# Kernel optimization log

Measured on AMD Instinct MI355X. Metric: run time of the kernel, lower is better.

Reference implementation:

```python
import jax, jax.numpy as jnp
import numpy as np

D_IN, L, D, K, N_CLASSES = 1024, 512, 384, 1, 2

def setup_inputs() -> dict:
    key = jax.random.key(0)
    ks = jax.random.split(key, 11)
    x = jax.random.normal(ks[0], (2, 40000, D_IN), dtype=jnp.float32)
    # Linear params stored as [in, out]; xavier-normal-ish scale
    def w(k, i, o):
        return jax.random.normal(k, (i, o), dtype=jnp.float32) * jnp.sqrt(2.0 / (i + o))
    return {
        "x": x,
        "Wf": w(ks[1], D_IN, L), "bf": jnp.zeros((L,), jnp.float32),
        "Wa": w(ks[2], L, D),    "ba": jnp.zeros((D,), jnp.float32),
        "Wb": w(ks[3], L, D),    "bb": jnp.zeros((D,), jnp.float32),
        "Wc": w(ks[4], D, K),    "bc": jnp.zeros((K,), jnp.float32),
        "Wcls": w(ks[5], L * K, N_CLASSES), "bcls": jnp.zeros((N_CLASSES,), jnp.float32),
    }

def reference(x, Wf, bf, Wa, ba, Wb, bb, Wc, bc, Wcls, bcls):
    # feature embed: Linear + ReLU  (mil_norm=None -> Identity norms)
    h = jax.nn.relu(jnp.einsum('bnd,de->bne', x, Wf) + bf)   # [B,N,L]
    # gated attention
    a = jnp.tanh(jnp.einsum('bnl,ld->bnd', h, Wa) + ba)      # [B,N,D]
    g = jax.nn.sigmoid(jnp.einsum('bnl,ld->bnd', h, Wb) + bb)
    s = jnp.einsum('bnd,dk->bnk', a * g, Wc) + bc            # [B,N,K]
    A = jax.nn.softmax(jnp.swapaxes(s, -1, -2), axis=-1)     # [B,K,N]
    pooled = jnp.einsum('bkn,bnl->bkl', A, h)                # [B,K,L]
    logits = jnp.squeeze(pooled, 1) @ Wcls + bcls            # [B,n_classes]
    return logits
```

## Files before the change

kernel.cpp:

```cpp
#include <hip/hip_runtime.h>
#include <cstdint>

typedef _Float16 f16;
typedef __attribute__((ext_vector_type(8))) _Float16 half8;
typedef __attribute__((ext_vector_type(4))) float floatx4;

#define NB      40000
#define M_TOTAL 80000
#define DIN     1024
#define LDIM    512
#define NBLK    1250
#define BPB     625
#define NCHUNK  16
#define RCHUNK  40

__global__ void k_prep(const float* __restrict__ Wf, const float* __restrict__ Wa,
                       const float* __restrict__ Wb,
                       f16* __restrict__ packedF, f16* __restrict__ packedAB)
{
    const int gid = blockIdx.x * 256 + threadIdx.x;
    if (gid < 65536) {
        const int lq = gid & 3, n = (gid >> 2) & 511, kb = gid >> 11;
        const int kbase = kb * 32 + lq * 8;
        half8 v;
        #pragma unroll
        for (int j = 0; j < 8; ++j) v[j] = (f16)Wf[(kbase + j) * 512 + n];
        *(half8*)&packedF[(long)gid * 8] = v;
    } else if (gid < 65536 + 49152) {
        const int g = gid - 65536;
        const int kb = g / 3072;
        const int rem = g - kb * 3072;
        const int c = rem >> 2, lq = rem & 3;
        const int d = ((c >> 5) << 4) + (c & 15);
        const int type = (c >> 4) & 1;
        const float* src = type ? Wb : Wa;
        const int kbase = kb * 32 + lq * 8;
        half8 v;
        #pragma unroll
        for (int j = 0; j < 8; ++j) v[j] = (f16)src[(kbase + j) * 384 + d];
        *(half8*)&packedAB[(long)g * 8] = v;
    }
}

__device__ inline float fast_sigmoid(float xx) { return 1.0f / (1.0f + __expf(-xx)); }
__device__ inline float fast_tanh(float xx) {
    float e = __expf(-2.0f * fabsf(xx));
    float r = (1.0f - e) / (1.0f + e);
    return xx >= 0.0f ? r : -r;
}

__global__ __launch_bounds__(512, 4) void k_fused(
    const float* __restrict__ x, const f16* __restrict__ packedF,
    const f16* __restrict__ packedAB,
    const float* __restrict__ bf, const float* __restrict__ ba,
    const float* __restrict__ bb, const float* __restrict__ Wc,
    float* __restrict__ partial_pool, float* __restrict__ partial_denom)
{
    __shared__ __align__(16) f16 Hs[64][512];
    __shared__ __align__(16) f16 As[64][128];
    float* wbuf = (float*)&As[0][0];

    const int tid = threadIdx.x;
    const int w = tid >> 6, lane = tid & 63, lr = lane & 15, lq = lane >> 4;
    const long row0 = (long)blockIdx.x * 64;
    const int sr = tid >> 3;
    const int sc = (tid & 7) << 4;
    const int swzw = (sr & 7) << 3;
    const int swzr = (lr & 7) << 3;
    const float* xp = x + (row0 + sr) * DIN + sc;

    floatx4 acc[4][4] = {};
    float4 xr0 = *(const float4*)xp;
    float4 xr1 = *(const float4*)(xp + 4);
    float4 xr2 = *(const float4*)(xp + 8);
    float4 xr3 = *(const float4*)(xp + 12);
    for (int kt = 0; kt < 8; ++kt) {
        if (kt) __syncthreads();
        {
            half8 v0, v1;
            v0[0]=(f16)xr0.x; v0[1]=(f16)xr0.y; v0[2]=(f16)xr0.z; v0[3]=(f16)xr0.w;
            v0[4]=(f16)xr1.x; v0[5]=(f16)xr1.y; v0[6]=(f16)xr1.z; v0[7]=(f16)xr1.w;
            v1[0]=(f16)xr2.x; v1[1]=(f16)xr2.y; v1[2]=(f16)xr2.z; v1[3]=(f16)xr2.w;
            v1[4]=(f16)xr3.x; v1[5]=(f16)xr3.y; v1[6]=(f16)xr3.z; v1[7]=(f16)xr3.w;
            *(half8*)&As[sr][sc ^ swzw] = v0;
            *(half8*)&As[sr][(sc + 8) ^ swzw] = v1;
        }
        __syncthreads();
        if (kt < 7) {
            const float* q = xp + (kt + 1) * 128;
            xr0 = *(const float4*)q;
            xr1 = *(const float4*)(q + 4);
            xr2 = *(const float4*)(q + 8);
            xr3 = *(const float4*)(q + 12);
        }
        #pragma unroll
        for (int kq = 0; kq < 4; ++kq) {
            const int kb = kt * 4 + kq;
            half8 bfr[4];
            #pragma unroll
            for (int tj = 0; tj < 4; ++tj)
                bfr[tj] = *(const half8*)&packedF[(long)((kb * 512 + w * 64 + tj * 16 + lr) << 5) + lq * 8];
            half8 af[4];
            #pragma unroll
            for (int ti = 0; ti < 4; ++ti)
                af[ti] = *(const half8*)&As[ti * 16 + lr][(kq * 32 + lq * 8) ^ swzr];
            #pragma unroll
            for (int tj = 0; tj < 4; ++tj)
                #pragma unroll
                for (int ti = 0; ti < 4; ++ti)
                    acc[ti][tj] = __builtin_amdgcn_mfma_f32_16x16x32_f16(af[ti], bfr[tj], acc[ti][tj], 0, 0, 0);
        }
    }
    #pragma unroll
    for (int tj = 0; tj < 4; ++tj) {
        const int col = w * 64 + tj * 16 + lr;
        const float bias = bf[col];
        #pragma unroll
        for (int ti = 0; ti < 4; ++ti)
            #pragma unroll
            for (int r = 0; r < 4; ++r) {
                const int row = ti * 16 + lq * 4 + r;
                Hs[row][col ^ ((row & 7) << 3)] = (f16)fmaxf(acc[ti][tj][r] + bias, 0.0f);
            }
    }
    __syncthreads();
    if (tid < 64) wbuf[tid] = 0.0f;
    __syncthreads();

    floatx4 acc2[4][6] = {};
    for (int kb = 0; kb < 16; ++kb) {
        half8 af[4];
        #pragma unroll
        for (int ti = 0; ti < 4; ++ti)
            af[ti] = *(const half8*)&Hs[ti * 16 + lr][(kb * 32 + lq * 8) ^ swzr];
        #pragma unroll
        for (int tj = 0; tj < 6; ++tj) {
            half8 bfr = *(const half8*)&packedAB[(long)((kb * 768 + w * 96 + tj * 16 + lr) << 5) + lq * 8];
            #pragma unroll
            for (int ti = 0; ti < 4; ++ti)
                acc2[ti][tj] = __builtin_amdgcn_mfma_f32_16x16x32_f16(af[ti], bfr, acc2[ti][tj], 0, 0, 0);
        }
    }
    float sp[4][4] = {};
    #pragma unroll
    for (int u = 0; u < 3; ++u) {
        const int d = w * 48 + u * 16 + lr;
        const float biasA = ba[d], biasB = bb[d], wcv = Wc[d];
        #pragma unroll
        for (int ti = 0; ti < 4; ++ti)
            #pragma unroll
            for (int r = 0; r < 4; ++r) {
                const float av = fast_tanh(acc2[ti][2 * u][r] + biasA);
                const float gv = fast_sigmoid(acc2[ti][2 * u + 1][r] + biasB);
                sp[ti][r] += av * gv * wcv;
            }
    }
    #pragma unroll
    for (int m = 1; m < 16; m <<= 1)
        #pragma unroll
        for (int ti = 0; ti < 4; ++ti)
            #pragma unroll
            for (int r = 0; r < 4; ++r)
                sp[ti][r] += __shfl_xor(sp[ti][r], m, 64);
    if (lr == 0) {
        #pragma unroll
        for (int ti = 0; ti < 4; ++ti)
            #pragma unroll
            for (int r = 0; r < 4; ++r)
                atomicAdd(&wbuf[ti * 16 + lq * 4 + r], sp[ti][r]);
    }
    __syncthreads();
    if (tid < 64) wbuf[tid] = __expf(wbuf[tid]);
    __syncthreads();

    {
        const int c = tid;
        float pacc = 0.0f;
        #pragma unroll 8
        for (int n = 0; n < 64; ++n)
            pacc += wbuf[n] * (float)Hs[n][c ^ ((n & 7) << 3)];
        partial_pool[(long)blockIdx.x * 512 + c] = pacc;
    }
    if (w == 0) {
        float dsum = wbuf[lane];
        #pragma unroll
        for (int o = 32; o > 0; o >>= 1) dsum += __shfl_xor(dsum, o, 64);
        if (lane == 0) partial_denom[blockIdx.x] = dsum;
    }
}

__global__ __launch_bounds__(512) void k_reduce1(
    const float* __restrict__ pp, const float* __restrict__ pd,
    float* __restrict__ pp2, float* __restrict__ pd2)
{
    __shared__ float dsh[8];
    const int b = blockIdx.x >> 4, chunk = blockIdx.x & 15;
    const int tid = threadIdx.x;
    const int r0 = chunk * RCHUNK;
    const int rows = (BPB - r0 < RCHUNK) ? (BPB - r0) : RCHUNK;
    const float* base = pp + ((long)b * BPB + r0) * 512 + tid;
    float acc = 0.0f;
    for (int i = 0; i < rows; ++i) acc += base[(long)i * 512];
    pp2[((long)b * NCHUNK + chunk) * 512 + tid] = acc;
    float d = 0.0f;
    for (int i = tid; i < rows; i += 512) d += pd[b * BPB + r0 + i];
    #pragma unroll
    for (int o = 32; o > 0; o >>= 1) d += __shfl_xor(d, o, 64);
    if ((tid & 63) == 0) dsh[tid >> 6] = d;
    __syncthreads();
    if (tid == 0)
        pd2[b * NCHUNK + chunk] = dsh[0] + dsh[1] + dsh[2] + dsh[3]
                                + dsh[4] + dsh[5] + dsh[6] + dsh[7];
}

__global__ __launch_bounds__(512) void k_reduce2(
    const float* __restrict__ pp2, const float* __restrict__ pd2,
    const float* __restrict__ Wcls, const float* __restrict__ bcls,
    float* __restrict__ out)
{
    __shared__ float pooled[512];
    __shared__ float dsh[8];
    const int b = blockIdx.x, tid = threadIdx.x;
    float acc = 0.0f;
    const float* base = pp2 + (long)b * NCHUNK * 512 + tid;
    #pragma unroll
    for (int i = 0; i < NCHUNK; ++i) acc += base[i * 512];
    pooled[tid] = acc;
    float d = (tid < NCHUNK) ? pd2[b * NCHUNK + tid] : 0.0f;
    #pragma unroll
    for (int o = 32; o > 0; o >>= 1) d += __shfl_xor(d, o, 64);
    if ((tid & 63) == 0) dsh[tid >> 6] = d;
    __syncthreads();
    const float denom = dsh[0] + dsh[1] + dsh[2] + dsh[3] + dsh[4] + dsh[5] + dsh[6] + dsh[7];
    if (tid < 128) {
        const int cls = tid >> 6, ln = tid & 63;
        float sum = 0.0f;
        #pragma unroll
        for (int t = 0; t < 8; ++t)
            sum += pooled[t * 64 + ln] * Wcls[(t * 64 + ln) * 2 + cls];
        #pragma unroll
        for (int o = 32; o > 0; o >>= 1) sum += __shfl_xor(sum, o, 64);
        if (ln == 0) out[b * 2 + cls] = sum / denom + bcls[cls];
    }
}

extern "C" void kernel_launch(void* const* d_in, const int* in_sizes, int n_in,
                              void* d_out, int out_size, void* d_ws, size_t ws_size,
                              hipStream_t stream)
{
    const float* x    = (const float*)d_in[0];
    const float* Wf   = (const float*)d_in[1];
    const float* bf   = (const float*)d_in[2];
    const float* Wa   = (const float*)d_in[3];
    const float* ba   = (const float*)d_in[4];
    const float* Wb   = (const float*)d_in[5];
    const float* bb   = (const float*)d_in[6];
    const float* Wc   = (const float*)d_in[7];
    const float* Wcls = (const float*)d_in[9];
    const float* bcls = (const float*)d_in[10];
    float* out = (float*)d_out;

    char* w = (char*)d_ws;
    f16*   packedF  = (f16*)(w);
    f16*   packedAB = (f16*)(w + 1048576);
    float* ppool    = (float*)(w + 1835008);
    float* pdenom   = (float*)(w + 4395008);
    float* pp2      = (float*)(w);
    float* pd2      = (float*)(w + 65536);

    k_prep   <<<448, 256, 0, stream>>>(Wf, Wa, Wb, packedF, packedAB);
    k_fused  <<<NBLK, 512, 0, stream>>>(x, packedF, packedAB, bf, ba, bb, Wc, ppool, pdenom);
    k_reduce1<<<32, 512, 0, stream>>>(ppool, pdenom, pp2, pd2);
    k_reduce2<<<2, 512, 0, stream>>>(pp2, pd2, Wcls, bcls, out);
}
```

Baseline: 690.3 us.

## Double fused-kernel row tile to 128 with 16 waves sharing weight fragments

Each fused block now handles 128 rows instead of 64, using 1024 threads arranged as a 2x8 grid of waves. Both row halves reuse the same column slices of the packed Wf/Wa/Wb weights, which cuts weight fetch traffic per row. Blocks are now mapped per batch, so each batch's final block has only 64 valid rows; it clamps loads and zeroes the weights of the missing rows. Pool and denominator partials are still written in 64-row halves so the reduction stage's layout is kept. Costs: LDS per block doubles to about 160KB, the grid is coarser with a possible tail effect, and register pressure under the new launch bounds rises.

```diff
diff --git a/kernel.cpp b/kernel.cpp
--- a/kernel.cpp
+++ b/kernel.cpp
@@ -6,11 +6,12 @@
 typedef __attribute__((ext_vector_type(4))) float floatx4;
 
 #define NB      40000
-#define M_TOTAL 80000
 #define DIN     1024
 #define LDIM    512
-#define NBLK    1250
-#define BPB     625
+#define BLKM    128
+#define BPBATCH 313
+#define GRID_F  626
+#define BPB     626
 #define NCHUNK  16
 #define RCHUNK  40
 
@@ -49,25 +50,33 @@
     return xx >= 0.0f ? r : -r;
 }
 
-__global__ __launch_bounds__(512, 4) void k_fused(
+__global__ __launch_bounds__(1024, 4) void k_fused(
     const float* __restrict__ x, const f16* __restrict__ packedF,
     const f16* __restrict__ packedAB,
     const float* __restrict__ bf, const float* __restrict__ ba,
     const float* __restrict__ bb, const float* __restrict__ Wc,
     float* __restrict__ partial_pool, float* __restrict__ partial_denom)
 {
-    __shared__ __align__(16) f16 Hs[64][512];
-    __shared__ __align__(16) f16 As[64][128];
+    __shared__ __align__(16) f16 Hs[128][512];
+    __shared__ __align__(16) f16 As[128][128];
     float* wbuf = (float*)&As[0][0];
 
     const int tid = threadIdx.x;
     const int w = tid >> 6, lane = tid & 63, lr = lane & 15, lq = lane >> 4;
-    const long row0 = (long)blockIdx.x * 64;
+    const int wm = w & 1;
+    const int wc = w >> 1;
+    const int bid = blockIdx.x;
+    const int batch = (bid >= BPBATCH) ? 1 : 0;
+    const int blk = bid - batch * BPBATCH;
+    const long row0 = (long)batch * NB + (long)blk * BLKM;
+    const int nvalid = (blk == BPBATCH - 1) ? 64 : BLKM;
+
     const int sr = tid >> 3;
     const int sc = (tid & 7) << 4;
     const int swzw = (sr & 7) << 3;
     const int swzr = (lr & 7) << 3;
-    const float* xp = x + (row0 + sr) * DIN + sc;
+    const long srow = row0 + (sr < nvalid ? sr : nvalid - 1);
+    const float* xp = x + srow * DIN + sc;
 
     floatx4 acc[4][4] = {};
     float4 xr0 = *(const float4*)xp;
@@ -99,11 +108,11 @@
             half8 bfr[4];
             #pragma unroll
             for (int tj = 0; tj < 4; ++tj)
-                bfr[tj] = *(const half8*)&packedF[(long)((kb * 512 + w * 64 + tj * 16 + lr) << 5) + lq * 8];
+                bfr[tj] = *(const half8*)&packedF[(long)((kb * 512 + wc * 64 + tj * 16 + lr) << 5) + lq * 8];
             half8 af[4];
             #pragma unroll
             for (int ti = 0; ti < 4; ++ti)
-                af[ti] = *(const half8*)&As[ti * 16 + lr][(kq * 32 + lq * 8) ^ swzr];
+                af[ti] = *(const half8*)&As[wm * 64 + ti * 16 + lr][(kq * 32 + lq * 8) ^ swzr];
             #pragma unroll
             for (int tj = 0; tj < 4; ++tj)
                 #pragma unroll
@@ -113,18 +122,18 @@
     }
     #pragma unroll
     for (int tj = 0; tj < 4; ++tj) {
-        const int col = w * 64 + tj * 16 + lr;
+        const int col = wc * 64 + tj * 16 + lr;
         const float bias = bf[col];
         #pragma unroll
         for (int ti = 0; ti < 4; ++ti)
             #pragma unroll
             for (int r = 0; r < 4; ++r) {
-                const int row = ti * 16 + lq * 4 + r;
+                const int row = wm * 64 + ti * 16 + lq * 4 + r;
                 Hs[row][col ^ ((row & 7) << 3)] = (f16)fmaxf(acc[ti][tj][r] + bias, 0.0f);
             }
     }
     __syncthreads();
-    if (tid < 64) wbuf[tid] = 0.0f;
+    if (tid < 128) wbuf[tid] = 0.0f;
     __syncthreads();
 
     floatx4 acc2[4][6] = {};
@@ -132,10 +141,10 @@
         half8 af[4];
         #pragma unroll
         for (int ti = 0; ti < 4; ++ti)
-            af[ti] = *(const half8*)&Hs[ti * 16 + lr][(kb * 32 + lq * 8) ^ swzr];
+            af[ti] = *(const half8*)&Hs[wm * 64 + ti * 16 + lr][(kb * 32 + lq * 8) ^ swzr];
         #pragma unroll
         for (int tj = 0; tj < 6; ++tj) {
-            half8 bfr = *(const half8*)&packedAB[(long)((kb * 768 + w * 96 + tj * 16 + lr) << 5) + lq * 8];
+            half8 bfr = *(const half8*)&packedAB[(long)((kb * 768 + wc * 96 + tj * 16 + lr) << 5) + lq * 8];
             #pragma unroll
             for (int ti = 0; ti < 4; ++ti)
                 acc2[ti][tj] = __builtin_amdgcn_mfma_f32_16x16x32_f16(af[ti], bfr, acc2[ti][tj], 0, 0, 0);
@@ -144,7 +153,7 @@
     float sp[4][4] = {};
     #pragma unroll
     for (int u = 0; u < 3; ++u) {
-        const int d = w * 48 + u * 16 + lr;
+        const int d = wc * 48 + u * 16 + lr;
         const float biasA = ba[d], biasB = bb[d], wcv = Wc[d];
         #pragma unroll
         for (int ti = 0; ti < 4; ++ti)
@@ -167,25 +176,28 @@
         for (int ti = 0; ti < 4; ++ti)
             #pragma unroll
             for (int r = 0; r < 4; ++r)
-                atomicAdd(&wbuf[ti * 16 + lq * 4 + r], sp[ti][r]);
-    }
-    __syncthreads();
-    if (tid < 64) wbuf[tid] = __expf(wbuf[tid]);
+                atomicAdd(&wbuf[wm * 64 + ti * 16 + lq * 4 + r], sp[ti][r]);
+    }
+    __syncthreads();
+    if (tid < 128)
+        wbuf[tid] = (tid < nvalid) ? __expf(wbuf[tid]) : 0.0f;
     __syncthreads();
 
     {
-        const int c = tid;
+        const int nh = tid >> 9;
+        const int c = tid & 511;
+        const int n0 = nh * 64;
         float pacc = 0.0f;
         #pragma unroll 8
-        for (int n = 0; n < 64; ++n)
+        for (int n = n0; n < n0 + 64; ++n)
             pacc += wbuf[n] * (float)Hs[n][c ^ ((n & 7) << 3)];
-        partial_pool[(long)blockIdx.x * 512 + c] = pacc;
-    }
-    if (w == 0) {
-        float dsum = wbuf[lane];
+        partial_pool[((long)bid * 2 + nh) * 512 + c] = pacc;
+    }
+    if (w < 2) {
+        float dsum = wbuf[w * 64 + lane];
         #pragma unroll
         for (int o = 32; o > 0; o >>= 1) dsum += __shfl_xor(dsum, o, 64);
-        if (lane == 0) partial_denom[blockIdx.x] = dsum;
+        if (lane == 0) partial_denom[bid * 2 + w] = dsum;
     }
 }
 
@@ -264,12 +276,12 @@
     f16*   packedF  = (f16*)(w);
     f16*   packedAB = (f16*)(w + 1048576);
     float* ppool    = (float*)(w + 1835008);
-    float* pdenom   = (float*)(w + 4395008);
+    float* pdenom   = (float*)(w + 4399104);
     float* pp2      = (float*)(w);
     float* pd2      = (float*)(w + 65536);
 
     k_prep   <<<448, 256, 0, stream>>>(Wf, Wa, Wb, packedF, packedAB);
-    k_fused  <<<NBLK, 512, 0, stream>>>(x, packedF, packedAB, bf, ba, bb, Wc, ppool, pdenom);
+    k_fused  <<<GRID_F, 1024, 0, stream>>>(x, packedF, packedAB, bf, ba, bb, Wc, ppool, pdenom);
     k_reduce1<<<32, 512, 0, stream>>>(ppool, pdenom, pp2, pd2);
     k_reduce2<<<2, 512, 0, stream>>>(pp2, pd2, Wcls, bcls, out);
 }
```

New measurement: 745.8 us. 1.08x slower.
